# Optimization experiments

Measured on AMD Instinct MI355X. Metric: run time of the kernel, lower is better.

Reference implementation:

```python
import jax, jax.numpy as jnp
import numpy as np

DIM = 1024
HEADS = 16


def setup_inputs() -> dict:
    key = jax.random.key(0)
    ks = jax.random.split(key, 8)
    B, Np, Nr, C = 4, 1024, 1024, DIM
    s = 0.02
    return {
        "Q": jax.random.normal(ks[0], (B, Np, C), jnp.float32),
        "K": jax.random.normal(ks[1], (B, Nr, C), jnp.float32),
        "Wq": jax.random.normal(ks[2], (C, C), jnp.float32) * s,
        "bq": jnp.zeros((C,), jnp.float32),
        "Wk": jax.random.normal(ks[3], (C, C), jnp.float32) * s,
        "bk": jnp.zeros((C,), jnp.float32),
        "Wv": jax.random.normal(ks[4], (C, C), jnp.float32) * s,
        "bv": jnp.zeros((C,), jnp.float32),
    }


def reference(Q, K, Wq, bq, Wk, bk, Wv, bv):
    B, Np, C = Q.shape
    Nr = K.shape[1]
    H = HEADS
    d = C // H
    # linear projections (torch Linear: x @ W.T + b)
    q = (Q @ Wq.T + bq).reshape(B, Np, H, d)
    k = (K @ Wk.T + bk).reshape(B, Nr, H, d)
    v = (K @ Wv.T + bv).reshape(B, Nr, H, d)
    # NOTE: original scales by sqrt(dim_V) (full dim), not sqrt(head_dim)
    scores = jnp.einsum("bqhd,bkhd->bhqk", q, k) / jnp.sqrt(jnp.float32(C))
    A = jax.nn.softmax(scores, axis=-1)  # [B,H,Np,Nr]
    O = jnp.einsum("bhqk,bkhd->bqhd", A, v).reshape(B, Np, C)
    # faithful reproduction of A.view(B,H,Np,N).mean(1) applied to a
    # head-major (H*B, Np, N) tensor: transpose to head-major, flat-reshape.
    A_avg = jnp.transpose(A, (1, 0, 2, 3)).reshape(B, H, Np, Nr).mean(axis=1)
    return (O, A_avg)
```

## Files before the change

### kernel.cpp

```cpp
#include <hip/hip_runtime.h>
#include <hip/hip_bf16.h>
#include <hip/hip_fp16.h>

typedef _Float16 f16x8 __attribute__((ext_vector_type(8)));
typedef _Float16 f16x4 __attribute__((ext_vector_type(4)));
typedef _Float16 f16x2 __attribute__((ext_vector_type(2)));
typedef float f32x4 __attribute__((ext_vector_type(4)));
typedef float f32x16 __attribute__((ext_vector_type(16)));
typedef unsigned int u32x4 __attribute__((ext_vector_type(4)));

#define MFMA16(a, b, c) __builtin_amdgcn_mfma_f32_16x16x32_f16(a, b, c, 0, 0, 0)
#define MFMA32(a, b, c) __builtin_amdgcn_mfma_f32_32x32x16_f16(a, b, c, 0, 0, 0)

#define C1 0.045084220027780106f

#define LGKM0_BARRIER do { \
    asm volatile("s_waitcnt lgkmcnt(0)" ::: "memory"); \
    __builtin_amdgcn_s_barrier(); \
} while (0)

__global__ void cvt_all(const float* __restrict__ Q, const float* __restrict__ K,
                        const float* __restrict__ Wq, const float* __restrict__ Wk,
                        const float* __restrict__ Wv, _Float16* __restrict__ dst) {
    int i = blockIdx.x * blockDim.x + threadIdx.x;
    const float* s;
    int off;
    if (i < 524288)       { s = Q;  off = 0;       }
    else if (i < 1048576) { s = K;  off = 524288;  }
    else if (i < 1179648) { s = Wq; off = 1048576; }
    else if (i < 1310720) { s = Wk; off = 1179648; }
    else                  { s = Wv; off = 1310720; }
    int j = i - off;
    float4 a = ((const float4*)s)[2 * j];
    float4 b = ((const float4*)s)[2 * j + 1];
    f16x8 h;
    h[0] = (_Float16)a.x; h[1] = (_Float16)a.y; h[2] = (_Float16)a.z; h[3] = (_Float16)a.w;
    h[4] = (_Float16)b.x; h[5] = (_Float16)b.y; h[6] = (_Float16)b.z; h[7] = (_Float16)b.w;
    ((f16x8*)dst)[i] = h;
}

__device__ __forceinline__ void gl_lds16(const void* g, void* l) {
    __builtin_amdgcn_global_load_lds(
        (const __attribute__((address_space(1))) void*)g,
        (__attribute__((address_space(3))) void*)l, 16, 0, 0);
}

__global__ __launch_bounds__(256) void proj_gemm(
    const _Float16* __restrict__ Qh, const _Float16* __restrict__ Kh,
    const _Float16* __restrict__ Wqh, const _Float16* __restrict__ Wkh,
    const _Float16* __restrict__ Wvh,
    const float* __restrict__ bq, const float* __restrict__ bk,
    const float* __restrict__ bv,
    _Float16* __restrict__ qT, _Float16* __restrict__ kT,
    _Float16* __restrict__ vT) {
    const int z = blockIdx.z;
    const _Float16* A = (z == 0) ? Qh : Kh;
    const _Float16* W = (z == 0) ? Wqh : (z == 1 ? Wkh : Wvh);
    const float* bias = (z == 0) ? bq : (z == 1 ? bk : bv);

    __shared__ __align__(16) _Float16 At[128 * 32];
    __shared__ __align__(16) _Float16 Bt[128 * 32];

    const int tid = threadIdx.x;
    const int w = tid >> 6, lane = tid & 63;
    const int g = lane >> 4, c = lane & 15;
    const int m0 = blockIdx.x * 128, n0 = blockIdx.y * 128;
    const int wm = (w & 1) * 64, wn = (w >> 1) * 64;
    const int srow = w * 32 + (lane >> 2);
    const int scol = (lane & 3) * 8;

    f32x4 acc[4][4] = {};

    for (int k0 = 0; k0 < 1024; k0 += 32) {
        __syncthreads();
#pragma unroll
        for (int t = 0; t < 2; ++t) {
            int r = srow + t * 16;
            gl_lds16(A + (size_t)(m0 + r) * 1024 + k0 + scol, &At[(w * 2 + t) * 512]);
            gl_lds16(W + (size_t)(n0 + r) * 1024 + k0 + scol, &Bt[(w * 2 + t) * 512]);
        }
        __syncthreads();
        f16x8 af[4], bf[4];
#pragma unroll
        for (int mt = 0; mt < 4; ++mt) af[mt] = *(const f16x8*)&At[(wm + mt * 16 + c) * 32 + g * 8];
#pragma unroll
        for (int nt = 0; nt < 4; ++nt) bf[nt] = *(const f16x8*)&Bt[(wn + nt * 16 + c) * 32 + g * 8];
#pragma unroll
        for (int mt = 0; mt < 4; ++mt)
#pragma unroll
            for (int nt = 0; nt < 4; ++nt)
                acc[mt][nt] = MFMA16(af[mt], bf[nt], acc[mt][nt]);
    }

    if (z == 0) {
#pragma unroll
        for (int mt = 0; mt < 4; ++mt)
#pragma unroll
            for (int nt = 0; nt < 4; ++nt) {
                int col = n0 + wn + nt * 16 + c;
                int hh = col >> 6, dd = col & 63;
                int dc = dd >> 4, hi2 = (dd >> 3) & 1, j = dd & 7;
                float bb = bias[col];
                int row0 = m0 + wm + mt * 16 + g * 4;
                int bbi = row0 >> 10;
                int qtq = (row0 >> 5) & 31;
                int q50 = row0 & 31;
                size_t base = ((((size_t)(bbi * 16 + hh) * 32 + qtq) * 4 + dc) * 32) * 16 +
                              hi2 * 8 + j;
#pragma unroll
                for (int i = 0; i < 4; ++i)
                    qT[base + (size_t)(q50 + i) * 16] = (_Float16)(acc[mt][nt][i] + bb);
            }
    } else if (z == 1) {
#pragma unroll
        for (int mt = 0; mt < 4; ++mt)
#pragma unroll
            for (int nt = 0; nt < 4; ++nt) {
                int col = n0 + wn + nt * 16 + c;
                int hh = col >> 6, dd = col & 63;
                int dc = dd >> 4, hi2 = (dd >> 3) & 1, j = dd & 7;
                float bb = bias[col];
                int row0 = m0 + wm + mt * 16 + g * 4;
                int bbi = row0 >> 10, nn = row0 & 1023;
                int wa = nn >> 7, kt = (nn >> 5) & 3, q50 = nn & 31;
                size_t base = (((((size_t)(bbi * 16 + hh) * 8 + wa) * 4 + kt) * 4 + dc) * 32) * 16 +
                              hi2 * 8 + j;
#pragma unroll
                for (int i = 0; i < 4; ++i)
                    kT[base + (size_t)(q50 + i) * 16] = (_Float16)(acc[mt][nt][i] + bb);
            }
    } else {
#pragma unroll
        for (int mt = 0; mt < 4; ++mt)
#pragma unroll
            for (int nt = 0; nt < 4; ++nt) {
                int col = n0 + wn + nt * 16 + c;
                int hh = col >> 6, dd = col & 63;
                int dh = dd >> 5, q5v = dd & 31;
                float bb = bias[col];
                int row0 = m0 + wm + mt * 16 + g * 4;
                int bbi = row0 >> 10, nn = row0 & 1023;
                int wa = nn >> 7, kt = (nn >> 5) & 3;
                int ks = (nn >> 4) & 1, hi2 = (nn >> 3) & 1, j0 = nn & 7;
                f16x4 pk;
#pragma unroll
                for (int i = 0; i < 4; ++i) pk[i] = (_Float16)(acc[mt][nt][i] + bb);
                size_t off = ((((((size_t)(bbi * 16 + hh) * 8 + wa) * 4 + kt) * 2 + dh) * 2 + ks) * 32 +
                              q5v) * 16 + hi2 * 8 + j0;
                *(f16x4*)&vT[off] = pk;
            }
    }
}

__global__ __launch_bounds__(512, 2) void attn(
    const _Float16* __restrict__ qT, const _Float16* __restrict__ kT,
    const _Float16* __restrict__ vT, float* __restrict__ O,
    _Float16* __restrict__ part0, _Float16* __restrict__ part1) {
    extern __shared__ __align__(16) char smem[];
    float* Obuf = (float*)smem;
    float* red_m = (float*)(smem + 69632);
    float* red_l = red_m + 256;

    const int tid = threadIdx.x, w = tid >> 6, lane = tid & 63;
    const int q5 = lane & 31, hi = lane >> 5;

    const int f = blockIdx.x;
    const int grp = f & 7, qt = f >> 3, q0 = qt * 32;
    const int chunk = grp & 1, b2 = grp >> 1;

    const int lofs = q5 * 16 + hi * 8;

    f16x8 bsel[2];
#pragma unroll
    for (int ks = 0; ks < 2; ++ks)
#pragma unroll
        for (int j = 0; j < 8; ++j)
            bsel[ks][j] = (hi * 8 + j == (q5 & 15) && (q5 >> 4) == ks)
                              ? (_Float16)1.0f : (_Float16)0.0f;

    f32x16 aacc[4] = {};

    f16x8 bK0[4], bK1[4], bV0[4], bV1[4], qf[4];

    {
        const int m0p = b2 * 16 + chunk * 8;
        const int head = (m0p & 3) * 16 + (m0p >> 2);
        const _Float16* kb = kT + ((size_t)head * 8 + w) * 8192 + lofs;
        const _Float16* vb = vT + ((size_t)head * 8 + w) * 8192 + lofs;
        const _Float16* qb = qT + ((size_t)head * 32 + qt) * 2048 + lofs;
#pragma unroll
        for (int dc = 0; dc < 4; ++dc) bK0[dc] = *(const f16x8*)(kb + dc * 512);
#pragma unroll
        for (int dc = 0; dc < 4; ++dc) bK1[dc] = *(const f16x8*)(kb + 2048 + dc * 512);
#pragma unroll
        for (int i = 0; i < 4; ++i) bV0[i] = *(const f16x8*)(vb + i * 512);
#pragma unroll
        for (int dc = 0; dc < 4; ++dc) qf[dc] = *(const f16x8*)(qb + dc * 512);
    }

#pragma unroll 1
    for (int p = 0; p < 8; ++p) {
        const int m = b2 * 16 + chunk * 8 + p;
        const int head = (m & 3) * 16 + (m >> 2);
        const _Float16* kb = kT + ((size_t)head * 8 + w) * 8192 + lofs;
        const _Float16* vb = vT + ((size_t)head * 8 + w) * 8192 + lofs;
        const int mn = m + 1;
        const int headn = (mn & 3) * 16 + (mn >> 2);
        const _Float16* kbn = kT + ((size_t)headn * 8 + w) * 8192 + lofs;
        const _Float16* vbn = vT + ((size_t)headn * 8 + w) * 8192 + lofs;
        const _Float16* qbn = qT + ((size_t)headn * 32 + qt) * 2048 + lofs;

        if (p) {
            int mp = m - 1; int bp = mp & 3, hp = mp >> 2;
            int qq = tid >> 4, dd = (tid & 15) * 4;
            f32x4 acc = {};
#pragma unroll
            for (int buf = 0; buf < 8; ++buf) {
                f32x4 v = *(f32x4*)&Obuf[buf * 2176 + qq * 68 + dd];
                acc += v;
            }
            *(f32x4*)(O + (size_t)bp * 1048576 + (size_t)(q0 + qq) * 1024 + hp * 64 + dd) = acc;
        }

        f32x16 s0 = {}, s1 = {}, s2 = {}, s3 = {};
#pragma unroll
        for (int dc = 0; dc < 4; ++dc) s0 = MFMA32(bK0[dc], qf[dc], s0);
#pragma unroll
        for (int dc = 0; dc < 4; ++dc) bK0[dc] = *(const f16x8*)(kb + 2 * 2048 + dc * 512);
#pragma unroll
        for (int dc = 0; dc < 4; ++dc) s1 = MFMA32(bK1[dc], qf[dc], s1);
#pragma unroll
        for (int dc = 0; dc < 4; ++dc) bK1[dc] = *(const f16x8*)(kb + 3 * 2048 + dc * 512);
#pragma unroll
        for (int dc = 0; dc < 4; ++dc) s2 = MFMA32(bK0[dc], qf[dc], s2);
#pragma unroll
        for (int i = 0; i < 4; ++i) bV1[i] = *(const f16x8*)(vb + 1 * 2048 + i * 512);
#pragma unroll
        for (int dc = 0; dc < 4; ++dc) s3 = MFMA32(bK1[dc], qf[dc], s3);

        float pm = -3.0e38f;
#pragma unroll
        for (int r = 0; r < 16; ++r) {
            pm = fmaxf(pm, s0[r]); pm = fmaxf(pm, s1[r]);
            pm = fmaxf(pm, s2[r]); pm = fmaxf(pm, s3[r]);
        }
        pm = fmaxf(pm, __shfl_xor(pm, 32, 64));
        float l = 0.f;
#pragma unroll
        for (int r = 0; r < 16; ++r) {
            float e0 = exp2f((s0[r] - pm) * C1); s0[r] = e0;
            float e1 = exp2f((s1[r] - pm) * C1); s1[r] = e1;
            float e2 = exp2f((s2[r] - pm) * C1); s2[r] = e2;
            float e3 = exp2f((s3[r] - pm) * C1); s3[r] = e3;
            l += (e0 + e1) + (e2 + e3);
        }
        l += __shfl_xor(l, 32, 64);
        if (hi == 0) { red_m[w * 32 + q5] = pm; red_l[w * 32 + q5] = l; }

        u32x4 av[4][2];
#define PACK_KT(SK, KT) { \
            unsigned pw[8]; \
            _Pragma("unroll") \
            for (int r2 = 0; r2 < 8; ++r2) { \
                f16x2 t2; \
                t2[0] = (_Float16)SK[2 * r2]; \
                t2[1] = (_Float16)SK[2 * r2 + 1]; \
                pw[r2] = __builtin_bit_cast(unsigned, t2); \
            } \
            unsigned recv[2][2]; \
            _Pragma("unroll") \
            for (int ks = 0; ks < 2; ++ks) \
                _Pragma("unroll") \
                for (int d = 0; d < 2; ++d) { \
                    unsigned send = hi ? pw[4 * ks + d] : pw[4 * ks + 2 + d]; \
                    recv[ks][d] = (unsigned)__shfl_xor((int)send, 32, 64); \
                } \
            _Pragma("unroll") \
            for (int ks = 0; ks < 2; ++ks) { \
                unsigned own0 = hi ? pw[4 * ks + 2] : pw[4 * ks + 0]; \
                unsigned own1 = hi ? pw[4 * ks + 3] : pw[4 * ks + 1]; \
                u32x4 a; \
                a[0] = hi ? recv[ks][0] : own0; \
                a[1] = hi ? recv[ks][1] : own1; \
                a[2] = hi ? own0 : recv[ks][0]; \
                a[3] = hi ? own1 : recv[ks][1]; \
                av[KT][ks] = a; \
            } \
        }
        PACK_KT(s0, 0)
        PACK_KT(s1, 1)
        PACK_KT(s2, 2)
        PACK_KT(s3, 3)
#undef PACK_KT

#pragma unroll
        for (int i = 0; i < 4; ++i) bK0[i] = *(const f16x8*)(vb + 2 * 2048 + i * 512);
#pragma unroll
        for (int i = 0; i < 4; ++i) bK1[i] = *(const f16x8*)(vb + 3 * 2048 + i * 512);

        LGKM0_BARRIER;

        float mr[4], lr[4], M = -3.0e38f;
#pragma unroll
        for (int t = 0; t < 4; ++t) {
            int wv = hi * 4 + t;
            mr[t] = red_m[wv * 32 + q5];
            lr[t] = red_l[wv * 32 + q5];
            M = fmaxf(M, mr[t]);
        }
        M = fmaxf(M, __shfl_xor(M, 32, 64));
        float L = 0.f;
#pragma unroll
        for (int t = 0; t < 4; ++t) L += lr[t] * exp2f((mr[t] - M) * C1);
        L += __shfl_xor(L, 32, 64);
        const float sc = exp2f((pm - M) * C1) / L;

        {
            const _Float16 sch = (_Float16)sc;
            f16x8 scv;
#pragma unroll
            for (int j2 = 0; j2 < 8; ++j2) scv[j2] = sch;
#pragma unroll
            for (int kt = 0; kt < 4; ++kt)
#pragma unroll
                for (int ks = 0; ks < 2; ++ks)
                    av[kt][ks] = __builtin_bit_cast(
                        u32x4, __builtin_bit_cast(f16x8, av[kt][ks]) * scv);
        }

        f32x16 o0 = {}, o1 = {};
#pragma unroll
        for (int ks = 0; ks < 2; ++ks) {
            f16x8 pa = __builtin_bit_cast(f16x8, av[0][ks]);
            o0 = MFMA32(pa, bV0[ks], o0);
            o1 = MFMA32(pa, bV0[2 + ks], o1);
        }
        aacc[0] = MFMA32(__builtin_bit_cast(f16x8, av[0][0]), bsel[0], aacc[0]);
        aacc[0] = MFMA32(__builtin_bit_cast(f16x8, av[0][1]), bsel[1], aacc[0]);
#pragma unroll
        for (int ks = 0; ks < 2; ++ks) {
            f16x8 pa = __builtin_bit_cast(f16x8, av[1][ks]);
            o0 = MFMA32(pa, bV1[ks], o0);
            o1 = MFMA32(pa, bV1[2 + ks], o1);
        }
        aacc[1] = MFMA32(__builtin_bit_cast(f16x8, av[1][0]), bsel[0], aacc[1]);
        aacc[1] = MFMA32(__builtin_bit_cast(f16x8, av[1][1]), bsel[1], aacc[1]);
#pragma unroll
        for (int ks = 0; ks < 2; ++ks) {
            f16x8 pa = __builtin_bit_cast(f16x8, av[2][ks]);
            o0 = MFMA32(pa, bK0[ks], o0);
            o1 = MFMA32(pa, bK0[2 + ks], o1);
        }
        aacc[2] = MFMA32(__builtin_bit_cast(f16x8, av[2][0]), bsel[0], aacc[2]);
        aacc[2] = MFMA32(__builtin_bit_cast(f16x8, av[2][1]), bsel[1], aacc[2]);
        if (p < 7) {
#pragma unroll
            for (int dc = 0; dc < 4; ++dc) bK0[dc] = *(const f16x8*)(kbn + dc * 512);
#pragma unroll
            for (int i = 0; i < 4; ++i) bV0[i] = *(const f16x8*)(vbn + i * 512);
        }
#pragma unroll
        for (int ks = 0; ks < 2; ++ks) {
            f16x8 pa = __builtin_bit_cast(f16x8, av[3][ks]);
            o0 = MFMA32(pa, bK1[ks], o0);
            o1 = MFMA32(pa, bK1[2 + ks], o1);
        }
        aacc[3] = MFMA32(__builtin_bit_cast(f16x8, av[3][0]), bsel[0], aacc[3]);
        aacc[3] = MFMA32(__builtin_bit_cast(f16x8, av[3][1]), bsel[1], aacc[3]);
        if (p < 7) {
#pragma unroll
            for (int dc = 0; dc < 4; ++dc) bK1[dc] = *(const f16x8*)(kbn + 2048 + dc * 512);
#pragma unroll
            for (int dc = 0; dc < 4; ++dc) qf[dc] = *(const f16x8*)(qbn + dc * 512);
        }

        float* ob = Obuf + w * 2176;
#pragma unroll
        for (int r = 0; r < 16; ++r) {
            int qq = (r & 3) + 8 * (r >> 2) + 4 * hi;
            ob[qq * 68 + q5] = o0[r];
            ob[qq * 68 + 32 + q5] = o1[r];
        }
        LGKM0_BARRIER;
    }

    {
        int mp = b2 * 16 + chunk * 8 + 7; int bp = mp & 3, hp = mp >> 2;
        int qq = tid >> 4, dd = (tid & 15) * 4;
        f32x4 acc = {};
#pragma unroll
        for (int buf = 0; buf < 8; ++buf) {
            f32x4 v = *(f32x4*)&Obuf[buf * 2176 + qq * 68 + dd];
            acc += v;
        }
        *(f32x4*)(O + (size_t)bp * 1048576 + (size_t)(q0 + qq) * 1024 + hp * 64 + dd) = acc;
    }

    {
        _Float16* pb = (chunk ? part1 : part0) + ((size_t)b2 * 1024 + q0) * 1024;
#pragma unroll
        for (int kt = 0; kt < 4; ++kt) {
            int k = w * 128 + kt * 32 + q5;
#pragma unroll
            for (int r = 0; r < 16; ++r) {
                int qq = (r & 3) + 8 * (r >> 2) + 4 * hi;
                pb[(size_t)qq * 1024 + k] = (_Float16)aacc[kt][r];
            }
        }
    }
}

__global__ void add_avg(const _Float16* __restrict__ p0,
                        const _Float16* __restrict__ p1,
                        float* __restrict__ out) {
    int i = blockIdx.x * blockDim.x + threadIdx.x;
    f16x8 a = ((const f16x8*)p0)[i];
    f16x8 b = ((const f16x8*)p1)[i];
    f32x4 r0, r1;
#pragma unroll
    for (int j = 0; j < 4; ++j) r0[j] = ((float)a[j] + (float)b[j]) * 0.0625f;
#pragma unroll
    for (int j = 0; j < 4; ++j) r1[j] = ((float)a[4 + j] + (float)b[4 + j]) * 0.0625f;
    *(f32x4*)&out[8 * i] = r0;
    *(f32x4*)&out[8 * i + 4] = r1;
}

extern "C" void kernel_launch(void* const* d_in, const int* in_sizes, int n_in,
                              void* d_out, int out_size, void* d_ws, size_t ws_size,
                              hipStream_t stream) {
    if (ws_size < ((size_t)46 << 20)) return;

    const float* Q  = (const float*)d_in[0];
    const float* K  = (const float*)d_in[1];
    const float* Wq = (const float*)d_in[2];
    const float* bq = (const float*)d_in[3];
    const float* Wk = (const float*)d_in[4];
    const float* bk = (const float*)d_in[5];
    const float* Wv = (const float*)d_in[6];
    const float* bv = (const float*)d_in[7];

    char* ws = (char*)d_ws;
    _Float16* Qh  = (_Float16*)(ws);
    _Float16* Kh  = (_Float16*)(ws + ((size_t)8 << 20));
    _Float16* Wqh = (_Float16*)(ws + ((size_t)16 << 20));
    _Float16* Wkh = (_Float16*)(ws + ((size_t)18 << 20));
    _Float16* Wvh = (_Float16*)(ws + ((size_t)20 << 20));
    _Float16* qT  = (_Float16*)(ws + ((size_t)22 << 20));
    _Float16* kT  = (_Float16*)(ws + ((size_t)30 << 20));
    _Float16* vT  = (_Float16*)(ws + ((size_t)38 << 20));
    _Float16* part0 = (_Float16*)(ws);
    _Float16* part1 = (_Float16*)(ws + ((size_t)8 << 20));

    float* O = (float*)d_out;
    float* Aavg = O + (size_t)4 * 1024 * 1024;

    cvt_all<<<dim3(1441792 / 256), 256, 0, stream>>>(Q, K, Wq, Wk, Wv, Qh);

    proj_gemm<<<dim3(32, 8, 3), 256, 0, stream>>>(Qh, Kh, Wqh, Wkh, Wvh,
                                                  bq, bk, bv, qT, kT, vT);

    const int SMEM = 71680;
    hipFuncSetAttribute((const void*)attn, hipFuncAttributeMaxDynamicSharedMemorySize, SMEM);
    attn<<<dim3(256), 512, SMEM, stream>>>(qT, kT, vT, O, part0, part1);

    add_avg<<<dim3(2048), 256, 0, stream>>>(part0, part1, Aavg);
}
```

Measured before the change: 127.3 us.

## Restage projection stores through LDS, prefold softmax scale, reorder attention PV pipeline

The q/k projection epilogue now stages each tile through a shared buffer so it can write 16-byte vectorised stores in the attention layout, and it folds the softmax scale constant into q so the exp2 calls no longer multiply by it. In the attention kernel, the PV product is now issued before the cross-wave max/sum reduction using unnormalised probabilities. The per-wave rescale factor is applied during the final O reduction through a new shared array. Register buffers are reorganised so all four K tiles are loaded together and V tiles prefetch during the QK MFMAs, and the f16 pack/swap uses cvt_pkrtz plus v_permlane32_swap. This overlaps MFMA work with the barrier and reduces shuffles, at the cost of extra shared memory, extra syncs in the projection epilogue, and possible overflow risk from unnormalised f16 probabilities.

```diff
diff --git a/kernel.cpp b/kernel.cpp
--- a/kernel.cpp
+++ b/kernel.cpp
@@ -60,6 +60,7 @@
 
     __shared__ __align__(16) _Float16 At[128 * 32];
     __shared__ __align__(16) _Float16 Bt[128 * 32];
+    __shared__ __align__(16) _Float16 Ct[32 * 132];
 
     const int tid = threadIdx.x;
     const int w = tid >> 6, lane = tid & 63;
@@ -92,43 +93,44 @@
                 acc[mt][nt] = MFMA16(af[mt], bf[nt], acc[mt][nt]);
     }
 
-    if (z == 0) {
-#pragma unroll
-        for (int mt = 0; mt < 4; ++mt)
+    if (z != 2) {
+        _Float16* T = (z == 0) ? qT : kT;
+        const float mulf = (z == 0) ? C1 : 1.0f;
+        __syncthreads();
+#pragma unroll
+        for (int mt = 0; mt < 4; ++mt) {
 #pragma unroll
             for (int nt = 0; nt < 4; ++nt) {
-                int col = n0 + wn + nt * 16 + c;
-                int hh = col >> 6, dd = col & 63;
-                int dc = dd >> 4, hi2 = (dd >> 3) & 1, j = dd & 7;
-                float bb = bias[col];
-                int row0 = m0 + wm + mt * 16 + g * 4;
-                int bbi = row0 >> 10;
-                int qtq = (row0 >> 5) & 31;
-                int q50 = row0 & 31;
-                size_t base = ((((size_t)(bbi * 16 + hh) * 32 + qtq) * 4 + dc) * 32) * 16 +
-                              hi2 * 8 + j;
-#pragma unroll
-                for (int i = 0; i < 4; ++i)
-                    qT[base + (size_t)(q50 + i) * 16] = (_Float16)(acc[mt][nt][i] + bb);
+                int colL = wn + nt * 16 + c;
+                float bb = bias[n0 + colL];
+#pragma unroll
+                for (int i = 0; i < 4; ++i) {
+                    int lr = (w & 1) * 16 + g * 4 + i;
+                    Ct[lr * 132 + colL] = (_Float16)((acc[mt][nt][i] + bb) * mulf);
+                }
             }
-    } else if (z == 1) {
-#pragma unroll
-        for (int mt = 0; mt < 4; ++mt)
-#pragma unroll
-            for (int nt = 0; nt < 4; ++nt) {
-                int col = n0 + wn + nt * 16 + c;
-                int hh = col >> 6, dd = col & 63;
-                int dc = dd >> 4, hi2 = (dd >> 3) & 1, j = dd & 7;
-                float bb = bias[col];
-                int row0 = m0 + wm + mt * 16 + g * 4;
-                int bbi = row0 >> 10, nn = row0 & 1023;
-                int wa = nn >> 7, kt = (nn >> 5) & 3, q50 = nn & 31;
-                size_t base = (((((size_t)(bbi * 16 + hh) * 8 + wa) * 4 + kt) * 4 + dc) * 32) * 16 +
-                              hi2 * 8 + j;
-#pragma unroll
-                for (int i = 0; i < 4; ++i)
-                    kT[base + (size_t)(q50 + i) * 16] = (_Float16)(acc[mt][nt][i] + bb);
+            __syncthreads();
+#pragma unroll
+            for (int rep = 0; rep < 2; ++rep) {
+                int eg = (tid >> 5) + rep * 8;
+                int r = tid & 31;
+                f16x8 vv = *(const f16x8*)&Ct[r * 132 + eg * 8];
+                int mrow = m0 + (r >> 4) * 64 + mt * 16 + (r & 15);
+                int colg = n0 + eg * 8;
+                int hh = colg >> 6, dsub = colg & 63;
+                int dc = dsub >> 4, hi2 = (dsub >> 3) & 1;
+                int bbi = mrow >> 10, nn = mrow & 1023;
+                size_t off;
+                if (z == 0)
+                    off = ((((size_t)(bbi * 16 + hh) * 32 + ((nn >> 5) & 31)) * 4 + dc) * 32 +
+                           (nn & 31)) * 16 + hi2 * 8;
+                else
+                    off = (((((size_t)(bbi * 16 + hh) * 8 + (nn >> 7)) * 4 + ((nn >> 5) & 3)) * 4 +
+                            dc) * 32 + (nn & 31)) * 16 + hi2 * 8;
+                *(f16x8*)&T[off] = vv;
             }
+            __syncthreads();
+        }
     } else {
 #pragma unroll
         for (int mt = 0; mt < 4; ++mt)
@@ -160,6 +162,7 @@
     float* Obuf = (float*)smem;
     float* red_m = (float*)(smem + 69632);
     float* red_l = red_m + 256;
+    float* sc_arr = red_l + 256;
 
     const int tid = threadIdx.x, w = tid >> 6, lane = tid & 63;
     const int q5 = lane & 31, hi = lane >> 5;
@@ -180,34 +183,31 @@
 
     f32x16 aacc[4] = {};
 
-    f16x8 bK0[4], bK1[4], bV0[4], bV1[4], qf[4];
+    f16x8 bA[4], bB[4], bC[4], bD[4], qf[4];
 
     {
         const int m0p = b2 * 16 + chunk * 8;
         const int head = (m0p & 3) * 16 + (m0p >> 2);
         const _Float16* kb = kT + ((size_t)head * 8 + w) * 8192 + lofs;
-        const _Float16* vb = vT + ((size_t)head * 8 + w) * 8192 + lofs;
         const _Float16* qb = qT + ((size_t)head * 32 + qt) * 2048 + lofs;
 #pragma unroll
-        for (int dc = 0; dc < 4; ++dc) bK0[dc] = *(const f16x8*)(kb + dc * 512);
-#pragma unroll
-        for (int dc = 0; dc < 4; ++dc) bK1[dc] = *(const f16x8*)(kb + 2048 + dc * 512);
-#pragma unroll
-        for (int i = 0; i < 4; ++i) bV0[i] = *(const f16x8*)(vb + i * 512);
-#pragma unroll
-        for (int dc = 0; dc < 4; ++dc) qf[dc] = *(const f16x8*)(qb + dc * 512);
+        for (int dc = 0; dc < 4; ++dc) {
+            bA[dc] = *(const f16x8*)(kb + dc * 512);
+            bB[dc] = *(const f16x8*)(kb + 2048 + dc * 512);
+            bC[dc] = *(const f16x8*)(kb + 4096 + dc * 512);
+            bD[dc] = *(const f16x8*)(kb + 6144 + dc * 512);
+            qf[dc] = *(const f16x8*)(qb + dc * 512);
+        }
     }
 
 #pragma unroll 1
     for (int p = 0; p < 8; ++p) {
         const int m = b2 * 16 + chunk * 8 + p;
         const int head = (m & 3) * 16 + (m >> 2);
-        const _Float16* kb = kT + ((size_t)head * 8 + w) * 8192 + lofs;
         const _Float16* vb = vT + ((size_t)head * 8 + w) * 8192 + lofs;
         const int mn = m + 1;
         const int headn = (mn & 3) * 16 + (mn >> 2);
         const _Float16* kbn = kT + ((size_t)headn * 8 + w) * 8192 + lofs;
-        const _Float16* vbn = vT + ((size_t)headn * 8 + w) * 8192 + lofs;
         const _Float16* qbn = qT + ((size_t)headn * 32 + qt) * 2048 + lofs;
 
         if (p) {
@@ -217,26 +217,30 @@
 #pragma unroll
             for (int buf = 0; buf < 8; ++buf) {
                 f32x4 v = *(f32x4*)&Obuf[buf * 2176 + qq * 68 + dd];
-                acc += v;
+                float fw = sc_arr[buf * 33 + qq];
+#pragma unroll
+                for (int j = 0; j < 4; ++j) acc[j] += v[j] * fw;
             }
             *(f32x4*)(O + (size_t)bp * 1048576 + (size_t)(q0 + qq) * 1024 + hp * 64 + dd) = acc;
         }
 
         f32x16 s0 = {}, s1 = {}, s2 = {}, s3 = {};
 #pragma unroll
-        for (int dc = 0; dc < 4; ++dc) s0 = MFMA32(bK0[dc], qf[dc], s0);
-#pragma unroll
-        for (int dc = 0; dc < 4; ++dc) bK0[dc] = *(const f16x8*)(kb + 2 * 2048 + dc * 512);
-#pragma unroll
-        for (int dc = 0; dc < 4; ++dc) s1 = MFMA32(bK1[dc], qf[dc], s1);
-#pragma unroll
-        for (int dc = 0; dc < 4; ++dc) bK1[dc] = *(const f16x8*)(kb + 3 * 2048 + dc * 512);
-#pragma unroll
-        for (int dc = 0; dc < 4; ++dc) s2 = MFMA32(bK0[dc], qf[dc], s2);
-#pragma unroll
-        for (int i = 0; i < 4; ++i) bV1[i] = *(const f16x8*)(vb + 1 * 2048 + i * 512);
-#pragma unroll
-        for (int dc = 0; dc < 4; ++dc) s3 = MFMA32(bK1[dc], qf[dc], s3);
+        for (int dc = 0; dc < 4; ++dc) s0 = MFMA32(bA[dc], qf[dc], s0);
+#pragma unroll
+        for (int i = 0; i < 4; ++i) bA[i] = *(const f16x8*)(vb + i * 512);
+#pragma unroll
+        for (int dc = 0; dc < 4; ++dc) s1 = MFMA32(bB[dc], qf[dc], s1);
+#pragma unroll
+        for (int i = 0; i < 4; ++i) bB[i] = *(const f16x8*)(vb + 2048 + i * 512);
+#pragma unroll
+        for (int dc = 0; dc < 4; ++dc) s2 = MFMA32(bC[dc], qf[dc], s2);
+#pragma unroll
+        for (int i = 0; i < 4; ++i) bC[i] = *(const f16x8*)(vb + 4096 + i * 512);
+#pragma unroll
+        for (int dc = 0; dc < 4; ++dc) s3 = MFMA32(bD[dc], qf[dc], s3);
+#pragma unroll
+        for (int i = 0; i < 4; ++i) bD[i] = *(const f16x8*)(vb + 6144 + i * 512);
 
         float pm = -3.0e38f;
 #pragma unroll
@@ -248,55 +252,75 @@
         float l = 0.f;
 #pragma unroll
         for (int r = 0; r < 16; ++r) {
-            float e0 = exp2f((s0[r] - pm) * C1); s0[r] = e0;
-            float e1 = exp2f((s1[r] - pm) * C1); s1[r] = e1;
-            float e2 = exp2f((s2[r] - pm) * C1); s2[r] = e2;
-            float e3 = exp2f((s3[r] - pm) * C1); s3[r] = e3;
+            float e0 = exp2f(s0[r] - pm); s0[r] = e0;
+            float e1 = exp2f(s1[r] - pm); s1[r] = e1;
+            float e2 = exp2f(s2[r] - pm); s2[r] = e2;
+            float e3 = exp2f(s3[r] - pm); s3[r] = e3;
             l += (e0 + e1) + (e2 + e3);
         }
         l += __shfl_xor(l, 32, 64);
         if (hi == 0) { red_m[w * 32 + q5] = pm; red_l[w * 32 + q5] = l; }
 
         u32x4 av[4][2];
-#define PACK_KT(SK, KT) { \
+#define PACK_KT(SK, KT) do { \
             unsigned pw[8]; \
             _Pragma("unroll") \
             for (int r2 = 0; r2 < 8; ++r2) { \
-                f16x2 t2; \
-                t2[0] = (_Float16)SK[2 * r2]; \
-                t2[1] = (_Float16)SK[2 * r2 + 1]; \
-                pw[r2] = __builtin_bit_cast(unsigned, t2); \
+                pw[r2] = __builtin_bit_cast( \
+                    unsigned, __builtin_amdgcn_cvt_pkrtz(SK[2 * r2], SK[2 * r2 + 1])); \
             } \
-            unsigned recv[2][2]; \
-            _Pragma("unroll") \
-            for (int ks = 0; ks < 2; ++ks) \
-                _Pragma("unroll") \
-                for (int d = 0; d < 2; ++d) { \
-                    unsigned send = hi ? pw[4 * ks + d] : pw[4 * ks + 2 + d]; \
-                    recv[ks][d] = (unsigned)__shfl_xor((int)send, 32, 64); \
-                } \
             _Pragma("unroll") \
             for (int ks = 0; ks < 2; ++ks) { \
-                unsigned own0 = hi ? pw[4 * ks + 2] : pw[4 * ks + 0]; \
-                unsigned own1 = hi ? pw[4 * ks + 3] : pw[4 * ks + 1]; \
-                u32x4 a; \
-                a[0] = hi ? recv[ks][0] : own0; \
-                a[1] = hi ? recv[ks][1] : own1; \
-                a[2] = hi ? own0 : recv[ks][0]; \
-                a[3] = hi ? own1 : recv[ks][1]; \
+                unsigned a0 = pw[4 * ks + 0], b0 = pw[4 * ks + 2]; \
+                unsigned a1 = pw[4 * ks + 1], b1 = pw[4 * ks + 3]; \
+                asm volatile("v_permlane32_swap_b32 %0, %1" : "+v"(a0), "+v"(b0)); \
+                asm volatile("v_permlane32_swap_b32 %0, %1" : "+v"(a1), "+v"(b1)); \
+                u32x4 a; a[0] = a0; a[1] = a1; a[2] = b0; a[3] = b1; \
                 av[KT][ks] = a; \
             } \
-        }
-        PACK_KT(s0, 0)
-        PACK_KT(s1, 1)
-        PACK_KT(s2, 2)
-        PACK_KT(s3, 3)
+        } while (0)
+        PACK_KT(s0, 0);
+        PACK_KT(s1, 1);
+        PACK_KT(s2, 2);
+        PACK_KT(s3, 3);
 #undef PACK_KT
 
-#pragma unroll
-        for (int i = 0; i < 4; ++i) bK0[i] = *(const f16x8*)(vb + 2 * 2048 + i * 512);
-#pragma unroll
-        for (int i = 0; i < 4; ++i) bK1[i] = *(const f16x8*)(vb + 3 * 2048 + i * 512);
+        f32x16 o0 = {}, o1 = {};
+#pragma unroll
+        for (int ks = 0; ks < 2; ++ks) {
+            f16x8 pa = __builtin_bit_cast(f16x8, av[0][ks]);
+            o0 = MFMA32(pa, bA[ks], o0);
+            o1 = MFMA32(pa, bA[2 + ks], o1);
+        }
+#pragma unroll
+        for (int dc = 0; dc < 4; ++dc) bA[dc] = *(const f16x8*)(kbn + dc * 512);
+#pragma unroll
+        for (int ks = 0; ks < 2; ++ks) {
+            f16x8 pa = __builtin_bit_cast(f16x8, av[1][ks]);
+            o0 = MFMA32(pa, bB[ks], o0);
+            o1 = MFMA32(pa, bB[2 + ks], o1);
+        }
+#pragma unroll
+        for (int dc = 0; dc < 4; ++dc) bB[dc] = *(const f16x8*)(kbn + 2048 + dc * 512);
+#pragma unroll
+        for (int ks = 0; ks < 2; ++ks) {
+            f16x8 pa = __builtin_bit_cast(f16x8, av[2][ks]);
+            o0 = MFMA32(pa, bC[ks], o0);
+            o1 = MFMA32(pa, bC[2 + ks], o1);
+        }
+#pragma unroll
+        for (int dc = 0; dc < 4; ++dc) bC[dc] = *(const f16x8*)(kbn + 4096 + dc * 512);
+#pragma unroll
+        for (int ks = 0; ks < 2; ++ks) {
+            f16x8 pa = __builtin_bit_cast(f16x8, av[3][ks]);
+            o0 = MFMA32(pa, bD[ks], o0);
+            o1 = MFMA32(pa, bD[2 + ks], o1);
+        }
+#pragma unroll
+        for (int dc = 0; dc < 4; ++dc) {
+            bD[dc] = *(const f16x8*)(kbn + 6144 + dc * 512);
+            qf[dc] = *(const f16x8*)(qbn + dc * 512);
+        }
 
         LGKM0_BARRIER;
 
@@ -311,9 +335,10 @@
         M = fmaxf(M, __shfl_xor(M, 32, 64));
         float L = 0.f;
 #pragma unroll
-        for (int t = 0; t < 4; ++t) L += lr[t] * exp2f((mr[t] - M) * C1);
+        for (int t = 0; t < 4; ++t) L += lr[t] * exp2f(mr[t] - M);
         L += __shfl_xor(L, 32, 64);
-        const float sc = exp2f((pm - M) * C1) / L;
+        const float sc = exp2f(pm - M) / L;
+        if (hi == 0) sc_arr[w * 33 + q5] = sc;
 
         {
             const _Float16 sch = (_Float16)sc;
@@ -327,51 +352,10 @@
                     av[kt][ks] = __builtin_bit_cast(
                         u32x4, __builtin_bit_cast(f16x8, av[kt][ks]) * scv);
         }
-
-        f32x16 o0 = {}, o1 = {};
-#pragma unroll
-        for (int ks = 0; ks < 2; ++ks) {
-            f16x8 pa = __builtin_bit_cast(f16x8, av[0][ks]);
-            o0 = MFMA32(pa, bV0[ks], o0);
-            o1 = MFMA32(pa, bV0[2 + ks], o1);
-        }
-        aacc[0] = MFMA32(__builtin_bit_cast(f16x8, av[0][0]), bsel[0], aacc[0]);
-        aacc[0] = MFMA32(__builtin_bit_cast(f16x8, av[0][1]), bsel[1], aacc[0]);
-#pragma unroll
-        for (int ks = 0; ks < 2; ++ks) {
-            f16x8 pa = __builtin_bit_cast(f16x8, av[1][ks]);
-            o0 = MFMA32(pa, bV1[ks], o0);
-            o1 = MFMA32(pa, bV1[2 + ks], o1);
-        }
-        aacc[1] = MFMA32(__builtin_bit_cast(f16x8, av[1][0]), bsel[0], aacc[1]);
-        aacc[1] = MFMA32(__builtin_bit_cast(f16x8, av[1][1]), bsel[1], aacc[1]);
-#pragma unroll
-        for (int ks = 0; ks < 2; ++ks) {
-            f16x8 pa = __builtin_bit_cast(f16x8, av[2][ks]);
-            o0 = MFMA32(pa, bK0[ks], o0);
-            o1 = MFMA32(pa, bK0[2 + ks], o1);
-        }
-        aacc[2] = MFMA32(__builtin_bit_cast(f16x8, av[2][0]), bsel[0], aacc[2]);
-        aacc[2] = MFMA32(__builtin_bit_cast(f16x8, av[2][1]), bsel[1], aacc[2]);
-        if (p < 7) {
-#pragma unroll
-            for (int dc = 0; dc < 4; ++dc) bK0[dc] = *(const f16x8*)(kbn + dc * 512);
-#pragma unroll
-            for (int i = 0; i < 4; ++i) bV0[i] = *(const f16x8*)(vbn + i * 512);
-        }
-#pragma unroll
-        for (int ks = 0; ks < 2; ++ks) {
-            f16x8 pa = __builtin_bit_cast(f16x8, av[3][ks]);
-            o0 = MFMA32(pa, bK1[ks], o0);
-            o1 = MFMA32(pa, bK1[2 + ks], o1);
-        }
-        aacc[3] = MFMA32(__builtin_bit_cast(f16x8, av[3][0]), bsel[0], aacc[3]);
-        aacc[3] = MFMA32(__builtin_bit_cast(f16x8, av[3][1]), bsel[1], aacc[3]);
-        if (p < 7) {
-#pragma unroll
-            for (int dc = 0; dc < 4; ++dc) bK1[dc] = *(const f16x8*)(kbn + 2048 + dc * 512);
-#pragma unroll
-            for (int dc = 0; dc < 4; ++dc) qf[dc] = *(const f16x8*)(qbn + dc * 512);
+#pragma unroll
+        for (int kt = 0; kt < 4; ++kt) {
+            aacc[kt] = MFMA32(__builtin_bit_cast(f16x8, av[kt][0]), bsel[0], aacc[kt]);
+            aacc[kt] = MFMA32(__builtin_bit_cast(f16x8, av[kt][1]), bsel[1], aacc[kt]);
         }
 
         float* ob = Obuf + w * 2176;
@@ -391,7 +375,9 @@
 #pragma unroll
         for (int buf = 0; buf < 8; ++buf) {
             f32x4 v = *(f32x4*)&Obuf[buf * 2176 + qq * 68 + dd];
-            acc += v;
+            float fw = sc_arr[buf * 33 + qq];
+#pragma unroll
+            for (int j = 0; j < 4; ++j) acc[j] += v[j] * fw;
         }
         *(f32x4*)(O + (size_t)bp * 1048576 + (size_t)(q0 + qq) * 1024 + hp * 64 + dd) = acc;
     }
@@ -459,7 +445,7 @@
     proj_gemm<<<dim3(32, 8, 3), 256, 0, stream>>>(Qh, Kh, Wqh, Wkh, Wvh,
                                                   bq, bk, bv, qT, kT, vT);
 
-    const int SMEM = 71680;
+    const int SMEM = 69632 + 1024 + 1024 + 8 * 33 * 4;
     hipFuncSetAttribute((const void*)attn, hipFuncAttributeMaxDynamicSharedMemorySize, SMEM);
     attn<<<dim3(256), 512, SMEM, stream>>>(qT, kT, vT, O, part0, part1);
 
```

Measured after the change: 105.4 us. 17.2% less time.
